# Performance work log

Hardware: AMD Instinct MI355X
Metric: run time of the kernel (lower is better)

## Reference

```python
import jax, jax.numpy as jnp
import numpy as np

NUM_GRAPHS = 2048


def gcn_conv(x, W, b, edge, N):
    # PyG GCNConv: x' = D^{-1/2} (A + I) D^{-1/2} (x W) + b
    src, dst = edge[0], edge[1]
    loop = jnp.arange(N, dtype=src.dtype)
    src = jnp.concatenate([src, loop])
    dst = jnp.concatenate([dst, loop])
    h = x @ W  # [N, out]
    deg = jax.ops.segment_sum(jnp.ones(dst.shape, x.dtype), dst, num_segments=N)
    dinv = jnp.where(deg > 0, jax.lax.rsqrt(deg), 0.0)
    norm = dinv[src] * dinv[dst]  # [E+N]
    out = jax.ops.segment_sum(h[src] * norm[:, None], dst, num_segments=N)
    return out + b


def pool_max_mean(x, batch, G):
    mx = jax.ops.segment_max(x, batch, num_segments=G)
    mx = jnp.where(jnp.isfinite(mx), mx, 0.0)  # guard empty segments
    s = jax.ops.segment_sum(x, batch, num_segments=G)
    cnt = jax.ops.segment_sum(jnp.ones((x.shape[0],), x.dtype), batch, num_segments=G)
    mean = s / jnp.maximum(cnt, 1.0)[:, None]
    return mx, mean


def setup_inputs() -> dict:
    key = jax.random.key(0)
    ks = jax.random.split(key, 20)
    F, CE, SE, DD = 64, 64, 32, 128
    Nc, Ec, Ns, Es = 100000, 1250000, 100000, 1250000

    def glorot(k, shape):
        fan_in, fan_out = shape[0], shape[1]
        lim = np.sqrt(6.0 / (fan_in + fan_out)).astype(np.float32)
        return jax.random.uniform(k, shape, jnp.float32, -lim, lim)

    inp = {
        "c": jax.random.normal(ks[0], (Nc, F), jnp.float32),
        "c_edge": jax.random.randint(ks[1], (2, Ec), 0, Nc),
        "c_batch": jnp.sort(jax.random.randint(ks[2], (Nc,), 0, NUM_GRAPHS)),
        "s": jax.random.normal(ks[3], (Ns, F), jnp.float32),
        "s_edge": jax.random.randint(ks[4], (2, Es), 0, Ns),
        "s_batch": jnp.sort(jax.random.randint(ks[5], (Ns,), 0, NUM_GRAPHS)),
        "Wc0": glorot(ks[6], (F, CE)), "bc0": jnp.zeros((CE,), jnp.float32),
        "Wc1": glorot(ks[7], (CE, CE)), "bc1": jnp.zeros((CE,), jnp.float32),
        "Wc2": glorot(ks[8], (CE, CE)), "bc2": jnp.zeros((CE,), jnp.float32),
        "Ws0": glorot(ks[9], (F, SE)), "bs0": jnp.zeros((SE,), jnp.float32),
        "Ws1": glorot(ks[10], (SE, SE)), "bs1": jnp.zeros((SE,), jnp.float32),
        "Ws2": glorot(ks[11], (SE, SE)), "bs2": jnp.zeros((SE,), jnp.float32),
        "Wd": glorot(ks[12], ((CE + SE) * 2, DD)), "bd": jnp.zeros((DD,), jnp.float32),
        "Wo": glorot(ks[13], (DD, 1)), "bo": jnp.zeros((1,), jnp.float32),
    }
    return inp


def reference(c, c_edge, c_batch, s, s_edge, s_batch,
              Wc0, bc0, Wc1, bc1, Wc2, bc2,
              Ws0, bs0, Ws1, bs1, Ws2, bs2,
              Wd, bd, Wo, bo):
    Nc, Ns = c.shape[0], s.shape[0]
    cro = jax.nn.relu(gcn_conv(c, Wc0, bc0, c_edge, Nc))
    cro = jax.nn.relu(gcn_conv(cro, Wc1, bc1, c_edge, Nc))
    cro = jax.nn.relu(gcn_conv(cro, Wc2, bc2, c_edge, Nc))
    solv = jax.nn.relu(gcn_conv(s, Ws0, bs0, s_edge, Ns))
    solv = jax.nn.relu(gcn_conv(solv, Ws1, bs1, s_edge, Ns))
    solv = jax.nn.relu(gcn_conv(solv, Ws2, bs2, s_edge, Ns))
    c_mx, c_mean = pool_max_mean(cro, c_batch, NUM_GRAPHS)
    s_mx, s_mean = pool_max_mean(solv, s_batch, NUM_GRAPHS)
    embed = jnp.concatenate([c_mx, c_mean, s_mx, s_mean], axis=1)  # [G, 192]
    dense = jax.nn.relu(embed @ Wd + bd)
    out = dense @ Wo + bo  # [G, 1]
    return out, embed
```

## Files before the change

### kernel.cpp

```cpp
#include <hip/hip_runtime.h>
#include <hip/hip_fp16.h>
#include <math.h>


static inline int cdiv(int a, int b) { return (a + b - 1) / b; }

#define BUCKET_CAP 8192
#define P1_CHUNK   4096

__global__ void zero_int(int* __restrict__ p, int n) {
    int i = blockIdx.x * blockDim.x + threadIdx.x;
    if (i < n) p[i] = 0;
}

__global__ __launch_bounds__(256) void p1_partition(const int* __restrict__ c_edge, int Ec,
                                                    const int* __restrict__ s_edge, int Es,
                                                    int Nc, int Etot, int nbuck,
                                                    int* __restrict__ bucket_fill,
                                                    unsigned* __restrict__ pk) {
    __shared__ unsigned       wbuf[P1_CHUNK];
    __shared__ unsigned short bbuf[P1_CHUNK];
    __shared__ int            hist[512];
    int e0 = blockIdx.x * P1_CHUNK;
    int n  = Etot - e0;
    if (n > P1_CHUNK) n = P1_CHUNK;
    for (int i = threadIdx.x; i < nbuck; i += 256) hist[i] = 0;
    __syncthreads();
    for (int i = threadIdx.x; i < n; i += 256) {
        int e = e0 + i, src, g;
        if (e < Ec) { src = c_edge[e]; g = c_edge[Ec + e]; }
        else        { int e2 = e - Ec; src = s_edge[e2]; g = Nc + s_edge[Es + e2]; }
        int b   = g >> 9;
        wbuf[i] = ((unsigned)(g & 511) << 17) | (unsigned)src;
        bbuf[i] = (unsigned short)b;
        atomicAdd(&hist[b], 1);
    }
    __syncthreads();
    for (int i = threadIdx.x; i < nbuck; i += 256) {
        int h = hist[i];
        hist[i] = h ? atomicAdd(&bucket_fill[i], h) : 0;
    }
    __syncthreads();
    for (int i = threadIdx.x; i < n; i += 256) {
        int b    = bbuf[i];
        int slot = atomicAdd(&hist[b], 1);
        if (slot < BUCKET_CAP) pk[(size_t)b * BUCKET_CAP + slot] = wbuf[i];
    }
}

__global__ __launch_bounds__(512) void p2_scanbuckets(const int* __restrict__ fill, int nbuck,
                                                      int* __restrict__ basearr,
                                                      int* __restrict__ off_all, int Ntot, int Etot) {
    __shared__ int sh[512];
    int v = (threadIdx.x < nbuck) ? fill[threadIdx.x] : 0;
    sh[threadIdx.x] = v;
    __syncthreads();
    for (int ofs = 1; ofs < 512; ofs <<= 1) {
        int t = (threadIdx.x >= ofs) ? sh[threadIdx.x - ofs] : 0;
        __syncthreads();
        sh[threadIdx.x] += t;
        __syncthreads();
    }
    if (threadIdx.x < nbuck) basearr[threadIdx.x] = sh[threadIdx.x] - v;
    if (threadIdx.x == 0) off_all[Ntot] = Etot;
}

__global__ __launch_bounds__(512) void p3_build(const unsigned* __restrict__ pk,
                                                const int* __restrict__ fillarr,
                                                const int* __restrict__ basearr,
                                                int Ntot,
                                                int* __restrict__ off_all,
                                                float* __restrict__ dinv,
                                                int* __restrict__ csr) {
    __shared__ int sh[512];
    int b    = blockIdx.x;
    int fill = fillarr[b];
    if (fill > BUCKET_CAP) fill = BUCKET_CAP;
    int base = basearr[b];
    const unsigned* reg = pk + (size_t)b * BUCKET_CAP;
    sh[threadIdx.x] = 0;
    __syncthreads();
    for (int i = threadIdx.x; i < fill; i += 512) atomicAdd(&sh[reg[i] >> 17], 1);
    __syncthreads();
    int cnt = sh[threadIdx.x];
    for (int ofs = 1; ofs < 512; ofs <<= 1) {
        int t = (threadIdx.x >= ofs) ? sh[threadIdx.x - ofs] : 0;
        __syncthreads();
        sh[threadIdx.x] += t;
        __syncthreads();
    }
    int excl = sh[threadIdx.x] - cnt;
    int node = b * 512 + threadIdx.x;
    if (node < Ntot) {
        off_all[node] = base + excl;
        dinv[node]    = rsqrtf((float)(cnt + 1));
    }
    __syncthreads();
    sh[threadIdx.x] = excl;
    __syncthreads();
    for (int i = threadIdx.x; i < fill; i += 512) {
        unsigned w    = reg[i];
        int      slot = atomicAdd(&sh[w >> 17], 1);
        csr[base + slot] = (int)(w & 0x1FFFFu);
    }
}

template <int K, int M>
__device__ void gemm_body(int bid, const float* __restrict__ X, const float* __restrict__ W,
                          const float* __restrict__ dinv, __half* __restrict__ H, int N,
                          char* smem_) {
    constexpr int CG = M / 4, RG = 256 / CG, RB = RG * 4;
    float* Xs = (float*)smem_;
    float* Ws = Xs + K * RB;
    const int t    = threadIdx.x;
    const int row0 = bid * RB;

    for (int idx = t; idx < K * M; idx += 256) Ws[idx] = W[idx];

    constexpr int NF4 = RB * K / 4;
    for (int idx = t; idx < NF4; idx += 256) {
        int row = idx / (K / 4), k4 = idx % (K / 4);
        float4 v = make_float4(0.f, 0.f, 0.f, 0.f);
        int gr = row0 + row;
        if (gr < N) v = *(const float4*)(X + (size_t)gr * K + k4 * 4);
        Xs[(k4 * 4 + 0) * RB + row] = v.x;
        Xs[(k4 * 4 + 1) * RB + row] = v.y;
        Xs[(k4 * 4 + 2) * RB + row] = v.z;
        Xs[(k4 * 4 + 3) * RB + row] = v.w;
    }
    __syncthreads();

    const int cc = t % CG, rr = t / CG;
    float acc[4][4] = {};
#pragma unroll 4
    for (int k = 0; k < K; k++) {
        float4 xv = *(const float4*)(Xs + k * RB + rr * 4);
        float4 wv = *(const float4*)(Ws + k * M + cc * 4);
        acc[0][0] += xv.x * wv.x; acc[0][1] += xv.x * wv.y; acc[0][2] += xv.x * wv.z; acc[0][3] += xv.x * wv.w;
        acc[1][0] += xv.y * wv.x; acc[1][1] += xv.y * wv.y; acc[1][2] += xv.y * wv.z; acc[1][3] += xv.y * wv.w;
        acc[2][0] += xv.z * wv.x; acc[2][1] += xv.z * wv.y; acc[2][2] += xv.z * wv.z; acc[2][3] += xv.z * wv.w;
        acc[3][0] += xv.w * wv.x; acc[3][1] += xv.w * wv.y; acc[3][2] += xv.w * wv.z; acc[3][3] += xv.w * wv.w;
    }

#pragma unroll
    for (int i = 0; i < 4; i++) {
        int gr = row0 + rr * 4 + i;
        if (gr < N) {
            float sc = dinv[gr];
            __half2* dp = (__half2*)(H + (size_t)gr * M + cc * 4);
            dp[0] = __floats2half2_rn(acc[i][0] * sc, acc[i][1] * sc);
            dp[1] = __floats2half2_rn(acc[i][2] * sc, acc[i][3] * sc);
        }
    }
}

__device__ __forceinline__ float4 load4h(const float2* __restrict__ base, size_t idx) {
    float2 r = base[idx];
    union { float2 f2; __half2 h2[2]; } u;
    u.f2 = r;
    float2 a = __half22float2(u.h2[0]);
    float2 b = __half22float2(u.h2[1]);
    return make_float4(a.x, a.y, b.x, b.y);
}

template <int M>
__device__ void agg_body(int bid, const __half* __restrict__ H, const int* __restrict__ off,
                         const int* __restrict__ csr, const float* __restrict__ dinv,
                         const float* __restrict__ b, float* __restrict__ out, int N) {
    constexpr int L   = M / 4;
    constexpr int NPW = 64 / L;
    int lane = threadIdx.x & 63;
    int wave = threadIdx.x >> 6;
    int fq   = lane & (L - 1);
    int sub  = lane / L;
    int node = (bid * 4 + wave) * NPW + sub;
    if (node >= N) return;
    const float2* H4 = (const float2*)H;
    int j0 = off[node], j1 = off[node + 1];
    float4 acc = load4h(H4, (size_t)node * L + fq);
    int j = j0;
    for (; j + 8 <= j1; j += 8) {
        int s0 = csr[j],     s1 = csr[j + 1], s2 = csr[j + 2], s3 = csr[j + 3];
        int s4 = csr[j + 4], s5 = csr[j + 5], s6 = csr[j + 6], s7 = csr[j + 7];
        float4 a0 = load4h(H4, (size_t)s0 * L + fq);
        float4 a1 = load4h(H4, (size_t)s1 * L + fq);
        float4 a2 = load4h(H4, (size_t)s2 * L + fq);
        float4 a3 = load4h(H4, (size_t)s3 * L + fq);
        float4 a4 = load4h(H4, (size_t)s4 * L + fq);
        float4 a5 = load4h(H4, (size_t)s5 * L + fq);
        float4 a6 = load4h(H4, (size_t)s6 * L + fq);
        float4 a7 = load4h(H4, (size_t)s7 * L + fq);
        acc.x += (a0.x + a1.x + a2.x + a3.x) + (a4.x + a5.x + a6.x + a7.x);
        acc.y += (a0.y + a1.y + a2.y + a3.y) + (a4.y + a5.y + a6.y + a7.y);
        acc.z += (a0.z + a1.z + a2.z + a3.z) + (a4.z + a5.z + a6.z + a7.z);
        acc.w += (a0.w + a1.w + a2.w + a3.w) + (a4.w + a5.w + a6.w + a7.w);
    }
    for (; j + 4 <= j1; j += 4) {
        int s0 = csr[j], s1 = csr[j + 1], s2 = csr[j + 2], s3 = csr[j + 3];
        float4 a0 = load4h(H4, (size_t)s0 * L + fq);
        float4 a1 = load4h(H4, (size_t)s1 * L + fq);
        float4 a2 = load4h(H4, (size_t)s2 * L + fq);
        float4 a3 = load4h(H4, (size_t)s3 * L + fq);
        acc.x += a0.x + a1.x + a2.x + a3.x;
        acc.y += a0.y + a1.y + a2.y + a3.y;
        acc.z += a0.z + a1.z + a2.z + a3.z;
        acc.w += a0.w + a1.w + a2.w + a3.w;
    }
    for (; j < j1; ++j) {
        float4 a = load4h(H4, (size_t)csr[j] * L + fq);
        acc.x += a.x; acc.y += a.y; acc.z += a.z; acc.w += a.w;
    }
    float  dv = dinv[node];
    float4 bb = ((const float4*)b)[fq];
    float  vx = dv * acc.x + bb.x;
    float  vy = dv * acc.y + bb.y;
    float  vz = dv * acc.z + bb.z;
    float  vw = dv * acc.w + bb.w;
    ((float4*)out)[(size_t)node * L + fq] =
        make_float4(vx > 0.f ? vx : 0.f, vy > 0.f ? vy : 0.f,
                    vz > 0.f ? vz : 0.f, vw > 0.f ? vw : 0.f);
}

__global__ __launch_bounds__(256) void gemmBoth0(const float* __restrict__ Xc, const float* __restrict__ Wc,
                                                 __half* __restrict__ cH, int Nc,
                                                 const float* __restrict__ Xs, const float* __restrict__ Ws,
                                                 __half* __restrict__ sH, int Ns,
                                                 const float* __restrict__ dinv_all, int nbC) {
    __shared__ __align__(16) char smem[40960];
    if (blockIdx.x < nbC) gemm_body<64, 64>(blockIdx.x, Xc, Wc, dinv_all, cH, Nc, smem);
    else                  gemm_body<64, 32>(blockIdx.x - nbC, Xs, Ws, dinv_all + Nc, sH, Ns, smem);
}

__global__ __launch_bounds__(256) void gemmBoth(const float* __restrict__ Xc, const float* __restrict__ Wc,
                                                __half* __restrict__ cH, int Nc,
                                                const float* __restrict__ Xs, const float* __restrict__ Ws,
                                                __half* __restrict__ sH, int Ns,
                                                const float* __restrict__ dinv_all, int nbC) {
    __shared__ __align__(16) char smem[32768];
    if (blockIdx.x < nbC) gemm_body<64, 64>(blockIdx.x, Xc, Wc, dinv_all, cH, Nc, smem);
    else                  gemm_body<32, 32>(blockIdx.x - nbC, Xs, Ws, dinv_all + Nc, sH, Ns, smem);
}

__global__ __launch_bounds__(256) void aggBoth(const __half* __restrict__ cH, const __half* __restrict__ sH,
                                               const int* __restrict__ off_all, const int* __restrict__ csr_all,
                                               const float* __restrict__ dinv_all,
                                               const float* __restrict__ bc, const float* __restrict__ bs,
                                               float* __restrict__ outc, float* __restrict__ outs,
                                               int Nc, int Ns, int nbC) {
    if (blockIdx.x < nbC) agg_body<64>(blockIdx.x, cH, off_all, csr_all, dinv_all, bc, outc, Nc);
    else                  agg_body<32>(blockIdx.x - nbC, sH, off_all + Nc, csr_all, dinv_all + Nc, bs, outs, Ns);
}

__device__ __forceinline__ int lbound(const int* __restrict__ a, int n, int key) {
    int lo = 0, hi = n;
    while (lo < hi) {
        int mid = (lo + hi) >> 1;
        if (a[mid] < key) lo = mid + 1; else hi = mid;
    }
    return lo;
}

template <int M>
__device__ void pool_body(int g, const float* __restrict__ X, const int* __restrict__ batch,
                          int N, float* __restrict__ embed, int baseOff) {
    int lo = lbound(batch, N, g);
    int hi = lbound(batch, N, g + 1);
    int f  = threadIdx.x;
    if (f >= M) return;
    float mx = 0.f, sm = 0.f;
    for (int i = lo; i < hi; ++i) {
        float v = X[(size_t)i * M + f];
        mx = fmaxf(mx, v);
        sm += v;
    }
    int   cn   = hi - lo;
    float mean = sm / (float)(cn > 0 ? cn : 1);
    embed[(size_t)g * 192 + baseOff + f]     = mx;
    embed[(size_t)g * 192 + baseOff + M + f] = mean;
}

__global__ __launch_bounds__(64) void poolBoth(const float* __restrict__ cX, const int* __restrict__ c_batch, int Nc,
                                               const float* __restrict__ sX, const int* __restrict__ s_batch, int Ns,
                                               float* __restrict__ embed, int G) {
    if (blockIdx.x < G) pool_body<64>(blockIdx.x, cX, c_batch, Nc, embed, 0);
    else                pool_body<32>(blockIdx.x - G, sX, s_batch, Ns, embed, 128);
}

__global__ __launch_bounds__(128) void dense_kernel(const float* __restrict__ embed,
                                                    const float* __restrict__ Wd,
                                                    const float* __restrict__ bd,
                                                    const float* __restrict__ Wo,
                                                    const float* __restrict__ bo,
                                                    float* __restrict__ out) {
    __shared__ float e[192];
    __shared__ float red[128];
    int g = blockIdx.x;
    for (int k = threadIdx.x; k < 192; k += 128) e[k] = embed[(size_t)g * 192 + k];
    __syncthreads();
    int   m   = threadIdx.x;
    float acc = bd[m];
    for (int k = 0; k < 192; ++k) acc += e[k] * Wd[k * 128 + m];
    float d = acc > 0.f ? acc : 0.f;
    red[m]  = d * Wo[m];
    __syncthreads();
    for (int ofs = 64; ofs > 0; ofs >>= 1) {
        if (m < ofs) red[m] += red[m + ofs];
        __syncthreads();
    }
    if (m == 0) out[g] = red[0] + bo[0];
}


extern "C" void kernel_launch(void* const* d_in, const int* in_sizes, int n_in,
                              void* d_out, int out_size, void* d_ws, size_t ws_size,
                              hipStream_t stream) {
    const float* c       = (const float*)d_in[0];
    const int*   c_edge  = (const int*)d_in[1];
    const int*   c_batch = (const int*)d_in[2];
    const float* s       = (const float*)d_in[3];
    const int*   s_edge  = (const int*)d_in[4];
    const int*   s_batch = (const int*)d_in[5];
    const float* Wc0 = (const float*)d_in[6],  *bc0 = (const float*)d_in[7];
    const float* Wc1 = (const float*)d_in[8],  *bc1 = (const float*)d_in[9];
    const float* Wc2 = (const float*)d_in[10], *bc2 = (const float*)d_in[11];
    const float* Ws0 = (const float*)d_in[12], *bs0 = (const float*)d_in[13];
    const float* Ws1 = (const float*)d_in[14], *bs1 = (const float*)d_in[15];
    const float* Ws2 = (const float*)d_in[16], *bs2 = (const float*)d_in[17];
    const float* Wd  = (const float*)d_in[18], *bd  = (const float*)d_in[19];
    const float* Wo  = (const float*)d_in[20], *bo  = (const float*)d_in[21];

    const int Nc = in_sizes[0] / 64;
    const int Ec = in_sizes[1] / 2;
    const int Ns = in_sizes[3] / 64;
    const int Es = in_sizes[4] / 2;
    const int G  = out_size / 193;
    const int Ntot  = Nc + Ns;
    const int Etot  = Ec + Es;
    const int nbuck = (Ntot + 511) >> 9;

    char* p = (char*)d_ws;
    auto  alloc = [&](size_t bytes) -> void* {
        void* r = (void*)p;
        p += (bytes + 255) & ~(size_t)255;
        return r;
    };
    int*      bucket_fill = (int*)alloc(512 * 4);
    int*      bucket_base = (int*)alloc(512 * 4);
    unsigned* pk          = (unsigned*)alloc((size_t)nbuck * BUCKET_CAP * 4);
    int*      off_all     = (int*)alloc(((size_t)Ntot + 1) * 4);
    int*      csr_all     = (int*)alloc((size_t)Etot * 4);
    float*    dinv_all    = (float*)alloc((size_t)Ntot * 4);
    float*    bufC        = (float*)alloc((size_t)Nc * 64 * 4);
    float*    bufS        = (float*)alloc((size_t)Ns * 32 * 4);
    __half*   cH          = (__half*)alloc((size_t)Nc * 64 * 2);
    __half*   sH          = (__half*)alloc((size_t)Ns * 32 * 2);

    float* outv  = (float*)d_out;
    float* embed = outv + G;

    const int nbGmC = cdiv(Nc, 64), nbGm0S = cdiv(Ns, 128), nbGmS = cdiv(Ns, 128);
    const int nbAgC = cdiv(Nc, 16), nbAgS  = cdiv(Ns, 32);

    zero_int<<<cdiv(nbuck, 256), 256, 0, stream>>>(bucket_fill, nbuck);
    p1_partition<<<cdiv(Etot, P1_CHUNK), 256, 0, stream>>>(c_edge, Ec, s_edge, Es,
                                                           Nc, Etot, nbuck, bucket_fill, pk);
    p2_scanbuckets<<<1, 512, 0, stream>>>(bucket_fill, nbuck, bucket_base, off_all, Ntot, Etot);
    p3_build<<<nbuck, 512, 0, stream>>>(pk, bucket_fill, bucket_base, Ntot,
                                        off_all, dinv_all, csr_all);

    gemmBoth0<<<nbGmC + nbGm0S, 256, 0, stream>>>(c, Wc0, cH, Nc, s, Ws0, sH, Ns, dinv_all, nbGmC);
    aggBoth<<<nbAgC + nbAgS, 256, 0, stream>>>(cH, sH, off_all, csr_all, dinv_all,
                                               bc0, bs0, bufC, bufS, Nc, Ns, nbAgC);
    gemmBoth<<<nbGmC + nbGmS, 256, 0, stream>>>(bufC, Wc1, cH, Nc, bufS, Ws1, sH, Ns, dinv_all, nbGmC);
    aggBoth<<<nbAgC + nbAgS, 256, 0, stream>>>(cH, sH, off_all, csr_all, dinv_all,
                                               bc1, bs1, bufC, bufS, Nc, Ns, nbAgC);
    gemmBoth<<<nbGmC + nbGmS, 256, 0, stream>>>(bufC, Wc2, cH, Nc, bufS, Ws2, sH, Ns, dinv_all, nbGmC);
    aggBoth<<<nbAgC + nbAgS, 256, 0, stream>>>(cH, sH, off_all, csr_all, dinv_all,
                                               bc2, bs2, bufC, bufS, Nc, Ns, nbAgC);

    poolBoth<<<2 * G, 64, 0, stream>>>(bufC, c_batch, Nc, bufS, s_batch, Ns, embed, G);

    dense_kernel<<<G, 128, 0, stream>>>(embed, Wd, bd, Wo, bo, outv);
}
```

Baseline: 434.8 us.

## Degree-sort aggregation nodes, store activations in fp16, pad smem, fuse pool+dense

Several changes land together. Nodes in each 512-node bucket are counting-sorted by in-degree into a permutation so that a wave's aggregation work is more balanced. Intermediate layer outputs are stored as fp16 instead of fp32, and the GEMM reads fp16 input, which cuts memory traffic. The transposed X tile in shared memory is padded to avoid bank conflicts, node ranges are padded to multiples of 512, and pooling is fused with the dense head into one kernel. In exchange, fp16 activations lose precision, and the fused pool runs with fewer threads per graph.

```diff
diff --git a/kernel.cpp b/kernel.cpp
--- a/kernel.cpp
+++ b/kernel.cpp
@@ -15,7 +15,7 @@
 
 __global__ __launch_bounds__(256) void p1_partition(const int* __restrict__ c_edge, int Ec,
                                                     const int* __restrict__ s_edge, int Es,
-                                                    int Nc, int Etot, int nbuck,
+                                                    int Nc_pad, int Etot, int nbuck,
                                                     int* __restrict__ bucket_fill,
                                                     unsigned* __restrict__ pk) {
     __shared__ unsigned       wbuf[P1_CHUNK];
@@ -29,7 +29,7 @@
     for (int i = threadIdx.x; i < n; i += 256) {
         int e = e0 + i, src, g;
         if (e < Ec) { src = c_edge[e]; g = c_edge[Ec + e]; }
-        else        { int e2 = e - Ec; src = s_edge[e2]; g = Nc + s_edge[Es + e2]; }
+        else        { int e2 = e - Ec; src = s_edge[e2]; g = Nc_pad + s_edge[Es + e2]; }
         int b   = g >> 9;
         wbuf[i] = ((unsigned)(g & 511) << 17) | (unsigned)src;
         bbuf[i] = (unsigned short)b;
@@ -50,7 +50,7 @@
 
 __global__ __launch_bounds__(512) void p2_scanbuckets(const int* __restrict__ fill, int nbuck,
                                                       int* __restrict__ basearr,
-                                                      int* __restrict__ off_all, int Ntot, int Etot) {
+                                                      int* __restrict__ off_all, int Ntot_pad, int Etot) {
     __shared__ int sh[512];
     int v = (threadIdx.x < nbuck) ? fill[threadIdx.x] : 0;
     sh[threadIdx.x] = v;
@@ -62,23 +62,25 @@
         __syncthreads();
     }
     if (threadIdx.x < nbuck) basearr[threadIdx.x] = sh[threadIdx.x] - v;
-    if (threadIdx.x == 0) off_all[Ntot] = Etot;
+    if (threadIdx.x == 0) off_all[Ntot_pad] = Etot;
 }
 
 __global__ __launch_bounds__(512) void p3_build(const unsigned* __restrict__ pk,
                                                 const int* __restrict__ fillarr,
                                                 const int* __restrict__ basearr,
-                                                int Ntot,
                                                 int* __restrict__ off_all,
                                                 float* __restrict__ dinv,
-                                                int* __restrict__ csr) {
+                                                int* __restrict__ csr,
+                                                int* __restrict__ perm) {
     __shared__ int sh[512];
+    __shared__ int dhist[64];
     int b    = blockIdx.x;
     int fill = fillarr[b];
     if (fill > BUCKET_CAP) fill = BUCKET_CAP;
     int base = basearr[b];
     const unsigned* reg = pk + (size_t)b * BUCKET_CAP;
     sh[threadIdx.x] = 0;
+    if (threadIdx.x < 64) dhist[threadIdx.x] = 0;
     __syncthreads();
     for (int i = threadIdx.x; i < fill; i += 512) atomicAdd(&sh[reg[i] >> 17], 1);
     __syncthreads();
@@ -91,10 +93,18 @@
     }
     int excl = sh[threadIdx.x] - cnt;
     int node = b * 512 + threadIdx.x;
-    if (node < Ntot) {
-        off_all[node] = base + excl;
-        dinv[node]    = rsqrtf((float)(cnt + 1));
-    }
+    off_all[node] = base + excl;
+    dinv[node]    = rsqrtf((float)(cnt + 1));
+    int bin = cnt < 63 ? cnt : 63;
+    atomicAdd(&dhist[bin], 1);
+    __syncthreads();
+    if (threadIdx.x == 0) {
+        int run = 0;
+        for (int i = 0; i < 64; ++i) { int v = dhist[i]; dhist[i] = run; run += v; }
+    }
+    __syncthreads();
+    int pslot = atomicAdd(&dhist[bin], 1);
+    perm[b * 512 + pslot] = node;
     __syncthreads();
     sh[threadIdx.x] = excl;
     __syncthreads();
@@ -105,28 +115,45 @@
     }
 }
 
-template <int K, int M>
-__device__ void gemm_body(int bid, const float* __restrict__ X, const float* __restrict__ W,
+template <int K, int M, typename TIN>
+__device__ void gemm_body(int bid, const TIN* __restrict__ X, const float* __restrict__ W,
                           const float* __restrict__ dinv, __half* __restrict__ H, int N,
                           char* smem_) {
-    constexpr int CG = M / 4, RG = 256 / CG, RB = RG * 4;
+    constexpr int CG = M / 4, RG = 256 / CG, RB = RG * 4, RBP = RB + 4;
     float* Xs = (float*)smem_;
-    float* Ws = Xs + K * RB;
+    float* Ws = Xs + K * RBP;
     const int t    = threadIdx.x;
     const int row0 = bid * RB;
 
     for (int idx = t; idx < K * M; idx += 256) Ws[idx] = W[idx];
 
-    constexpr int NF4 = RB * K / 4;
-    for (int idx = t; idx < NF4; idx += 256) {
-        int row = idx / (K / 4), k4 = idx % (K / 4);
-        float4 v = make_float4(0.f, 0.f, 0.f, 0.f);
-        int gr = row0 + row;
-        if (gr < N) v = *(const float4*)(X + (size_t)gr * K + k4 * 4);
-        Xs[(k4 * 4 + 0) * RB + row] = v.x;
-        Xs[(k4 * 4 + 1) * RB + row] = v.y;
-        Xs[(k4 * 4 + 2) * RB + row] = v.z;
-        Xs[(k4 * 4 + 3) * RB + row] = v.w;
+    if constexpr (sizeof(TIN) == 4) {
+        constexpr int NF4 = RB * K / 4;
+        for (int idx = t; idx < NF4; idx += 256) {
+            int row = idx / (K / 4), k4 = idx % (K / 4);
+            float4 v = make_float4(0.f, 0.f, 0.f, 0.f);
+            int gr = row0 + row;
+            if (gr < N) v = *(const float4*)((const float*)X + (size_t)gr * K + k4 * 4);
+            Xs[(k4 * 4 + 0) * RBP + row] = v.x;
+            Xs[(k4 * 4 + 1) * RBP + row] = v.y;
+            Xs[(k4 * 4 + 2) * RBP + row] = v.z;
+            Xs[(k4 * 4 + 3) * RBP + row] = v.w;
+        }
+    } else {
+        constexpr int NF8 = RB * K / 8;
+        for (int idx = t; idx < NF8; idx += 256) {
+            int row = idx / (K / 8), k8 = idx % (K / 8);
+            int gr = row0 + row;
+            union { float4 f4; __half2 h2[4]; } u;
+            u.f4 = make_float4(0.f, 0.f, 0.f, 0.f);
+            if (gr < N) u.f4 = *(const float4*)((const __half*)X + (size_t)gr * K + k8 * 8);
+#pragma unroll
+            for (int q = 0; q < 4; ++q) {
+                float2 pq = __half22float2(u.h2[q]);
+                Xs[(k8 * 8 + 2 * q + 0) * RBP + row] = pq.x;
+                Xs[(k8 * 8 + 2 * q + 1) * RBP + row] = pq.y;
+            }
+        }
     }
     __syncthreads();
 
@@ -134,7 +161,7 @@
     float acc[4][4] = {};
 #pragma unroll 4
     for (int k = 0; k < K; k++) {
-        float4 xv = *(const float4*)(Xs + k * RB + rr * 4);
+        float4 xv = *(const float4*)(Xs + k * RBP + rr * 4);
         float4 wv = *(const float4*)(Ws + k * M + cc * 4);
         acc[0][0] += xv.x * wv.x; acc[0][1] += xv.x * wv.y; acc[0][2] += xv.x * wv.z; acc[0][3] += xv.x * wv.w;
         acc[1][0] += xv.y * wv.x; acc[1][1] += xv.y * wv.y; acc[1][2] += xv.y * wv.z; acc[1][3] += xv.y * wv.w;
@@ -164,19 +191,23 @@
 }
 
 template <int M>
-__device__ void agg_body(int bid, const __half* __restrict__ H, const int* __restrict__ off,
-                         const int* __restrict__ csr, const float* __restrict__ dinv,
-                         const float* __restrict__ b, float* __restrict__ out, int N) {
+__device__ void agg_body(int bid, const __half* __restrict__ H,
+                         const int* __restrict__ off_g, const int* __restrict__ csr,
+                         const float* __restrict__ dinv_g, const float* __restrict__ b,
+                         __half* __restrict__ out,
+                         const int* __restrict__ permSide, int idBase, int Nloc) {
     constexpr int L   = M / 4;
     constexpr int NPW = 64 / L;
     int lane = threadIdx.x & 63;
     int wave = threadIdx.x >> 6;
     int fq   = lane & (L - 1);
     int sub  = lane / L;
-    int node = (bid * 4 + wave) * NPW + sub;
-    if (node >= N) return;
+    int slot = (bid * 4 + wave) * NPW + sub;
+    int g    = permSide[slot];
+    int node = g - idBase;
+    if (node >= Nloc) return;
     const float2* H4 = (const float2*)H;
-    int j0 = off[node], j1 = off[node + 1];
+    int j0 = off_g[g], j1 = off_g[g + 1];
     float4 acc = load4h(H4, (size_t)node * L + fq);
     int j = j0;
     for (; j + 8 <= j1; j += 8) {
@@ -210,45 +241,50 @@
         float4 a = load4h(H4, (size_t)csr[j] * L + fq);
         acc.x += a.x; acc.y += a.y; acc.z += a.z; acc.w += a.w;
     }
-    float  dv = dinv[node];
+    float  dv = dinv_g[g];
     float4 bb = ((const float4*)b)[fq];
     float  vx = dv * acc.x + bb.x;
     float  vy = dv * acc.y + bb.y;
     float  vz = dv * acc.z + bb.z;
     float  vw = dv * acc.w + bb.w;
-    ((float4*)out)[(size_t)node * L + fq] =
-        make_float4(vx > 0.f ? vx : 0.f, vy > 0.f ? vy : 0.f,
-                    vz > 0.f ? vz : 0.f, vw > 0.f ? vw : 0.f);
+    union { float2 f2; __half2 h2[2]; } o;
+    o.h2[0] = __floats2half2_rn(vx > 0.f ? vx : 0.f, vy > 0.f ? vy : 0.f);
+    o.h2[1] = __floats2half2_rn(vz > 0.f ? vz : 0.f, vw > 0.f ? vw : 0.f);
+    ((float2*)out)[(size_t)node * L + fq] = o.f2;
 }
 
 __global__ __launch_bounds__(256) void gemmBoth0(const float* __restrict__ Xc, const float* __restrict__ Wc,
                                                  __half* __restrict__ cH, int Nc,
                                                  const float* __restrict__ Xs, const float* __restrict__ Ws,
                                                  __half* __restrict__ sH, int Ns,
-                                                 const float* __restrict__ dinv_all, int nbC) {
-    __shared__ __align__(16) char smem[40960];
-    if (blockIdx.x < nbC) gemm_body<64, 64>(blockIdx.x, Xc, Wc, dinv_all, cH, Nc, smem);
-    else                  gemm_body<64, 32>(blockIdx.x - nbC, Xs, Ws, dinv_all + Nc, sH, Ns, smem);
-}
-
-__global__ __launch_bounds__(256) void gemmBoth(const float* __restrict__ Xc, const float* __restrict__ Wc,
+                                                 const float* __restrict__ dinv_all, int Nc_pad, int nbC) {
+    __shared__ __align__(16) char smem[41984];
+    if (blockIdx.x < nbC) gemm_body<64, 64, float>(blockIdx.x, Xc, Wc, dinv_all, cH, Nc, smem);
+    else                  gemm_body<64, 32, float>(blockIdx.x - nbC, Xs, Ws, dinv_all + Nc_pad, sH, Ns, smem);
+}
+
+__global__ __launch_bounds__(256) void gemmBoth(const __half* __restrict__ Xc, const float* __restrict__ Wc,
                                                 __half* __restrict__ cH, int Nc,
-                                                const float* __restrict__ Xs, const float* __restrict__ Ws,
+                                                const __half* __restrict__ Xs, const float* __restrict__ Ws,
                                                 __half* __restrict__ sH, int Ns,
-                                                const float* __restrict__ dinv_all, int nbC) {
-    __shared__ __align__(16) char smem[32768];
-    if (blockIdx.x < nbC) gemm_body<64, 64>(blockIdx.x, Xc, Wc, dinv_all, cH, Nc, smem);
-    else                  gemm_body<32, 32>(blockIdx.x - nbC, Xs, Ws, dinv_all + Nc, sH, Ns, smem);
+                                                const float* __restrict__ dinv_all, int Nc_pad, int nbC) {
+    __shared__ __align__(16) char smem[34816];
+    if (blockIdx.x < nbC) gemm_body<64, 64, __half>(blockIdx.x, Xc, Wc, dinv_all, cH, Nc, smem);
+    else                  gemm_body<32, 32, __half>(blockIdx.x - nbC, Xs, Ws, dinv_all + Nc_pad, sH, Ns, smem);
 }
 
 __global__ __launch_bounds__(256) void aggBoth(const __half* __restrict__ cH, const __half* __restrict__ sH,
                                                const int* __restrict__ off_all, const int* __restrict__ csr_all,
                                                const float* __restrict__ dinv_all,
                                                const float* __restrict__ bc, const float* __restrict__ bs,
-                                               float* __restrict__ outc, float* __restrict__ outs,
-                                               int Nc, int Ns, int nbC) {
-    if (blockIdx.x < nbC) agg_body<64>(blockIdx.x, cH, off_all, csr_all, dinv_all, bc, outc, Nc);
-    else                  agg_body<32>(blockIdx.x - nbC, sH, off_all + Nc, csr_all, dinv_all + Nc, bs, outs, Ns);
+                                               __half* __restrict__ outc, __half* __restrict__ outs,
+                                               const int* __restrict__ perm,
+                                               int Nc, int Ns, int Nc_pad, int nbC) {
+    if (blockIdx.x < nbC)
+        agg_body<64>(blockIdx.x, cH, off_all, csr_all, dinv_all, bc, outc, perm, 0, Nc);
+    else
+        agg_body<32>(blockIdx.x - nbC, sH, off_all, csr_all, dinv_all, bs, outs,
+                     perm + Nc_pad, Nc_pad, Ns);
 }
 
 __device__ __forceinline__ int lbound(const int* __restrict__ a, int n, int key) {
@@ -260,54 +296,48 @@
     return lo;
 }
 
-template <int M>
-__device__ void pool_body(int g, const float* __restrict__ X, const int* __restrict__ batch,
-                          int N, float* __restrict__ embed, int baseOff) {
-    int lo = lbound(batch, N, g);
-    int hi = lbound(batch, N, g + 1);
-    int f  = threadIdx.x;
-    if (f >= M) return;
-    float mx = 0.f, sm = 0.f;
-    for (int i = lo; i < hi; ++i) {
-        float v = X[(size_t)i * M + f];
-        mx = fmaxf(mx, v);
-        sm += v;
-    }
-    int   cn   = hi - lo;
-    float mean = sm / (float)(cn > 0 ? cn : 1);
-    embed[(size_t)g * 192 + baseOff + f]     = mx;
-    embed[(size_t)g * 192 + baseOff + M + f] = mean;
-}
-
-__global__ __launch_bounds__(64) void poolBoth(const float* __restrict__ cX, const int* __restrict__ c_batch, int Nc,
-                                               const float* __restrict__ sX, const int* __restrict__ s_batch, int Ns,
-                                               float* __restrict__ embed, int G) {
-    if (blockIdx.x < G) pool_body<64>(blockIdx.x, cX, c_batch, Nc, embed, 0);
-    else                pool_body<32>(blockIdx.x - G, sX, s_batch, Ns, embed, 128);
-}
-
-__global__ __launch_bounds__(128) void dense_kernel(const float* __restrict__ embed,
-                                                    const float* __restrict__ Wd,
-                                                    const float* __restrict__ bd,
-                                                    const float* __restrict__ Wo,
-                                                    const float* __restrict__ bo,
-                                                    float* __restrict__ out) {
+__global__ __launch_bounds__(128) void poolDense(const __half* __restrict__ cX, const int* __restrict__ c_batch, int Nc,
+                                                 const __half* __restrict__ sX, const int* __restrict__ s_batch, int Ns,
+                                                 const float* __restrict__ Wd, const float* __restrict__ bd,
+                                                 const float* __restrict__ Wo, const float* __restrict__ bo,
+                                                 float* __restrict__ outv, float* __restrict__ embed) {
     __shared__ float e[192];
     __shared__ float red[128];
-    int g = blockIdx.x;
-    for (int k = threadIdx.x; k < 192; k += 128) e[k] = embed[(size_t)g * 192 + k];
-    __syncthreads();
-    int   m   = threadIdx.x;
-    float acc = bd[m];
-    for (int k = 0; k < 192; ++k) acc += e[k] * Wd[k * 128 + m];
+    int g = blockIdx.x, t = threadIdx.x;
+    if (t < 64) {
+        int lo = lbound(c_batch, Nc, g), hi = lbound(c_batch, Nc, g + 1);
+        float mx = 0.f, sm = 0.f;
+        for (int i = lo; i < hi; ++i) {
+            float v = __half2float(cX[(size_t)i * 64 + t]);
+            mx = fmaxf(mx, v); sm += v;
+        }
+        int cn = hi - lo;
+        e[t]      = mx;
+        e[64 + t] = sm / (float)(cn > 0 ? cn : 1);
+    } else if (t < 96) {
+        int f  = t - 64;
+        int lo = lbound(s_batch, Ns, g), hi = lbound(s_batch, Ns, g + 1);
+        float mx = 0.f, sm = 0.f;
+        for (int i = lo; i < hi; ++i) {
+            float v = __half2float(sX[(size_t)i * 32 + f]);
+            mx = fmaxf(mx, v); sm += v;
+        }
+        int cn = hi - lo;
+        e[128 + f] = mx;
+        e[160 + f] = sm / (float)(cn > 0 ? cn : 1);
+    }
+    __syncthreads();
+    for (int k = t; k < 192; k += 128) embed[(size_t)g * 192 + k] = e[k];
+    float acc = bd[t];
+    for (int k = 0; k < 192; ++k) acc += e[k] * Wd[k * 128 + t];
     float d = acc > 0.f ? acc : 0.f;
-    red[m]  = d * Wo[m];
+    red[t]  = d * Wo[t];
     __syncthreads();
     for (int ofs = 64; ofs > 0; ofs >>= 1) {
-        if (m < ofs) red[m] += red[m + ofs];
+        if (t < ofs) red[t] += red[t + ofs];
         __syncthreads();
     }
-    if (m == 0) out[g] = red[0] + bo[0];
+    if (t == 0) outv[g] = red[0] + bo[0];
 }
 
 
@@ -334,9 +364,11 @@
     const int Ns = in_sizes[3] / 64;
     const int Es = in_sizes[4] / 2;
     const int G  = out_size / 193;
-    const int Ntot  = Nc + Ns;
-    const int Etot  = Ec + Es;
-    const int nbuck = (Ntot + 511) >> 9;
+    const int Nc_pad   = cdiv(Nc, 512) * 512;
+    const int Ns_pad   = cdiv(Ns, 512) * 512;
+    const int Ntot_pad = Nc_pad + Ns_pad;
+    const int Etot     = Ec + Es;
+    const int nbuck    = Ntot_pad >> 9;
 
     char* p = (char*)d_ws;
     auto  alloc = [&](size_t bytes) -> void* {
@@ -347,11 +379,12 @@
     int*      bucket_fill = (int*)alloc(512 * 4);
     int*      bucket_base = (int*)alloc(512 * 4);
     unsigned* pk          = (unsigned*)alloc((size_t)nbuck * BUCKET_CAP * 4);
-    int*      off_all     = (int*)alloc(((size_t)Ntot + 1) * 4);
+    int*      off_all     = (int*)alloc(((size_t)Ntot_pad + 1) * 4);
     int*      csr_all     = (int*)alloc((size_t)Etot * 4);
-    float*    dinv_all    = (float*)alloc((size_t)Ntot * 4);
-    float*    bufC        = (float*)alloc((size_t)Nc * 64 * 4);
-    float*    bufS        = (float*)alloc((size_t)Ns * 32 * 4);
+    float*    dinv_all    = (float*)alloc((size_t)Ntot_pad * 4);
+    int*      perm        = (int*)alloc((size_t)Ntot_pad * 4);
+    __half*   bufC        = (__half*)alloc((size_t)Nc * 64 * 2);
+    __half*   bufS        = (__half*)alloc((size_t)Ns * 32 * 2);
     __half*   cH          = (__half*)alloc((size_t)Nc * 64 * 2);
     __half*   sH          = (__half*)alloc((size_t)Ns * 32 * 2);
 
@@ -359,26 +392,28 @@
     float* embed = outv + G;
 
     const int nbGmC = cdiv(Nc, 64), nbGm0S = cdiv(Ns, 128), nbGmS = cdiv(Ns, 128);
-    const int nbAgC = cdiv(Nc, 16), nbAgS  = cdiv(Ns, 32);
+    const int nbAgC = Nc_pad / 16,  nbAgS  = Ns_pad / 32;
 
     zero_int<<<cdiv(nbuck, 256), 256, 0, stream>>>(bucket_fill, nbuck);
     p1_partition<<<cdiv(Etot, P1_CHUNK), 256, 0, stream>>>(c_edge, Ec, s_edge, Es,
-                                                           Nc, Etot, nbuck, bucket_fill, pk);
-    p2_scanbuckets<<<1, 512, 0, stream>>>(bucket_fill, nbuck, bucket_base, off_all, Ntot, Etot);
-    p3_build<<<nbuck, 512, 0, stream>>>(pk, bucket_fill, bucket_base, Ntot,
-                                        off_all, dinv_all, csr_all);
-
-    gemmBoth0<<<nbGmC + nbGm0S, 256, 0, stream>>>(c, Wc0, cH, Nc, s, Ws0, sH, Ns, dinv_all, nbGmC);
+                                                           Nc_pad, Etot, nbuck, bucket_fill, pk);
+    p2_scanbuckets<<<1, 512, 0, stream>>>(bucket_fill, nbuck, bucket_base, off_all, Ntot_pad, Etot);
+    p3_build<<<nbuck, 512, 0, stream>>>(pk, bucket_fill, bucket_base,
+                                        off_all, dinv_all, csr_all, perm);
+
+    gemmBoth0<<<nbGmC + nbGm0S, 256, 0, stream>>>(c, Wc0, cH, Nc, s, Ws0, sH, Ns,
+                                                  dinv_all, Nc_pad, nbGmC);
     aggBoth<<<nbAgC + nbAgS, 256, 0, stream>>>(cH, sH, off_all, csr_all, dinv_all,
-                                               bc0, bs0, bufC, bufS, Nc, Ns, nbAgC);
-    gemmBoth<<<nbGmC + nbGmS, 256, 0, stream>>>(bufC, Wc1, cH, Nc, bufS, Ws1, sH, Ns, dinv_all, nbGmC);
+                                               bc0, bs0, bufC, bufS, perm, Nc, Ns, Nc_pad, nbAgC);
+    gemmBoth<<<nbGmC + nbGmS, 256, 0, stream>>>(bufC, Wc1, cH, Nc, bufS, Ws1, sH, Ns,
+                                                dinv_all, Nc_pad, nbGmC);
     aggBoth<<<nbAgC + nbAgS, 256, 0, stream>>>(cH, sH, off_all, csr_all, dinv_all,
-                                               bc1, bs1, bufC, bufS, Nc, Ns, nbAgC);
-    gemmBoth<<<nbGmC + nbGmS, 256, 0, stream>>>(bufC, Wc2, cH, Nc, bufS, Ws2, sH, Ns, dinv_all, nbGmC);
+                                               bc1, bs1, bufC, bufS, perm, Nc, Ns, Nc_pad, nbAgC);
+    gemmBoth<<<nbGmC + nbGmS, 256, 0, stream>>>(bufC, Wc2, cH, Nc, bufS, Ws2, sH, Ns,
+                                                dinv_all, Nc_pad, nbGmC);
     aggBoth<<<nbAgC + nbAgS, 256, 0, stream>>>(cH, sH, off_all, csr_all, dinv_all,
-                                               bc2, bs2, bufC, bufS, Nc, Ns, nbAgC);
-
-    poolBoth<<<2 * G, 64, 0, stream>>>(bufC, c_batch, Nc, bufS, s_batch, Ns, embed, G);
-
-    dense_kernel<<<G, 128, 0, stream>>>(embed, Wd, bd, Wo, bo, outv);
-}
+                                               bc2, bs2, bufC, bufS, perm, Nc, Ns, Nc_pad, nbAgC);
+
+    poolDense<<<G, 128, 0, stream>>>(bufC, c_batch, Nc, bufS, s_batch, Ns,
+                                     Wd, bd, Wo, bo, outv, embed);
+}
```

Result: slower. 445.9 us (+2.6%).
